# Optimization experiments

Measured on AMD Instinct MI355X. Metric: run time of the kernel, lower is better.

Reference implementation:

```python
import jax, jax.numpy as jnp
import numpy as np

B, L, E, H = 4, 2048, 1024, 16
D = E // H  # head_dim = 64
NEG_INF = -1e9


def _rope(x):
    # x: [B, L, H, D]; standard rotate-half RoPE over head_dim
    seq = x.shape[1]
    inv_freq = 1.0 / (10000.0 ** (jnp.arange(0, D, 2, dtype=jnp.float32) / D))  # [D/2]
    ang = jnp.arange(seq, dtype=jnp.float32)[:, None] * inv_freq               # [L, D/2]
    cos = jnp.concatenate([jnp.cos(ang), jnp.cos(ang)], axis=-1)[None, :, None, :]
    sin = jnp.concatenate([jnp.sin(ang), jnp.sin(ang)], axis=-1)[None, :, None, :]
    x1, x2 = jnp.split(x, 2, axis=-1)
    rot = jnp.concatenate([-x2, x1], axis=-1)
    return x * cos + rot * sin


def setup_inputs() -> dict:
    key = jax.random.key(0)
    ks = jax.random.split(key, 12)
    xavier = lambda k: jax.random.uniform(k, (E, E), jnp.float32,
                                          -np.sqrt(6.0 / (E + E)), np.sqrt(6.0 / (E + E)))
    return {
        "query": jax.random.normal(ks[0], (B, L, E), jnp.float32),
        "key": jax.random.normal(ks[1], (B, L, E), jnp.float32),
        "value": jax.random.normal(ks[2], (B, L, E), jnp.float32),
        "wq": xavier(ks[3]), "bq": jnp.zeros((E,), jnp.float32),
        "wk": xavier(ks[4]), "bk": jnp.zeros((E,), jnp.float32),
        "wv": xavier(ks[5]), "bv": jnp.zeros((E,), jnp.float32),
        "wo": xavier(ks[6]), "bo": jnp.zeros((E,), jnp.float32),
        "key_padding_mask": jax.random.randint(ks[7], (B, L), 0, 2).astype(bool),
    }


def reference(query, key, value, wq, bq, wk, bk, wv, bv, wo, bo, key_padding_mask):
    b, ql = query.shape[0], query.shape[1]
    sl = key.shape[1]
    q = (query @ wq.T + bq).reshape(b, ql, H, D)
    k = (key @ wk.T + bk).reshape(b, sl, H, D)
    v = (value @ wv.T + bv).reshape(b, sl, H, D)
    q = _rope(q)
    k = _rope(k)
    # causal mask (is_causal=True, attn_mask=None path) + key padding mask, additive
    causal = jnp.where(jnp.triu(jnp.ones((ql, sl), bool), k=1), NEG_INF, 0.0)  # [L, L]
    kpm = jnp.where(key_padding_mask[:, None, None, :], NEG_INF, 0.0)          # [B,1,1,S]
    mask = causal[None, None, :, :] + kpm
    scores = jnp.einsum("bqhd,bkhd->bhqk", q, k) / np.sqrt(D) + mask
    attn = jax.nn.softmax(scores, axis=-1)
    out = jnp.einsum("bhqk,bkhd->bqhd", attn, v).reshape(b, ql, E)
    return out @ wo.T + bo
```

## Files before the change

### kernel.cpp

```cpp
#include <hip/hip_runtime.h>

typedef unsigned short u16;
typedef unsigned int   u32;

using bf16x8 = __attribute__((ext_vector_type(8))) __bf16;
using f32x4  = __attribute__((ext_vector_type(4))) float;
using f32x16 = __attribute__((ext_vector_type(16))) float;
using u32x4  = __attribute__((ext_vector_type(4))) u32;

#define DEV static __device__ __forceinline__
#define GP(p) (const __attribute__((address_space(1))) void*)(p)
#define LP(p) (__attribute__((address_space(3))) void*)(p)
#define WAITB(N) asm volatile("s_waitcnt vmcnt(" N ")\n\ts_barrier" ::: "memory")
#define WAITVM(N) do{ asm volatile("s_waitcnt vmcnt(" N ")" ::: "memory"); \
                      __builtin_amdgcn_sched_barrier(0); }while(0)
#define LGKMB asm volatile("s_waitcnt lgkmcnt(0)\n\ts_barrier" ::: "memory")

DEV u16 f2bf(float f){
  u32 u = __builtin_bit_cast(u32, f);
  u32 r = u + 0x7fffu + ((u>>16)&1u);
  return (u16)(r>>16);
}
DEV float bcf(u32 x){ return __builtin_bit_cast(float, x); }
DEV bf16x8 as_bf(uint4 v){ return __builtin_bit_cast(bf16x8, v); }
DEV u32 cvt_pk(float lo, float hi){
  u32 r;
  asm("v_cvt_pk_bf16_f32 %0, %1, %2" : "=v"(r) : "v"(lo), "v"(hi));
  return r;
}
DEV void plswap(u32 &a, u32 &b){
  auto r = __builtin_amdgcn_permlane32_swap((int)a, (int)b, false, false);
  a = (u32)r[0]; b = (u32)r[1];
}
DEV float fexp2(float x){ float r; asm("v_exp_f32 %0, %1" : "=v"(r) : "v"(x)); return r; }
DEV float max3f(float a, float b, float c){
  float r; asm("v_max3_f32 %0, %1, %2, %3" : "=v"(r) : "v"(a), "v"(b), "v"(c)); return r;
}
DEV float fractf_(float x){ float r; asm("v_fract_f32 %0, %1" : "=v"(r) : "v"(x)); return r; }
DEV float sinrev(float f){ float r; asm("v_sin_f32 %0, %1" : "=v"(r) : "v"(f)); return r; }
DEV float cosrev(float f){ float r; asm("v_cos_f32 %0, %1" : "=v"(r) : "v"(f)); return r; }

constexpr int CB = 4, CL = 2048, CE = 1024, CH = 16, CD = 64;
constexpr int CM = CB*CL;
constexpr float LOG2E  = 1.44269504088896f;
constexpr float NEGBIG = -1.44269504e9f;
constexpr float INV2PI = 0.15915494309189535f;

__global__ void mask_kernel(const void* __restrict__ mask, float* __restrict__ maskf){
  __shared__ int a_gt1, a_badf, a_oddnz, a_evennz;
  if (threadIdx.x==0){ a_gt1=0; a_badf=0; a_oddnz=0; a_evennz=0; }
  __syncthreads();
  const u32* w = (const u32*)mask;
  int gt1=0, badf=0, oddnz=0, evennz=0;
  for (int i=threadIdx.x; i<2048; i+=256){
    u32 v = w[i];
    if (v > 1u) gt1 = 1;
    if (v != 0u && v != 0x3f800000u) badf = 1;
    if (v != 0u){ if (i & 1) oddnz = 1; else evennz = 1; }
  }
  if (gt1) atomicOr(&a_gt1,1);
  if (badf) atomicOr(&a_badf,1);
  if (oddnz) atomicOr(&a_oddnz,1);
  if (evennz) atomicOr(&a_evennz,1);
  __syncthreads();
  int mode;
  if (!a_gt1)           mode = (!a_oddnz && a_evennz) ? 3 : 0;
  else if (!a_badf)     mode = 1;
  else                  mode = 2;
  int i = blockIdx.x*blockDim.x + threadIdx.x;
  int v;
  if      (mode==0) v = ((const int*)mask)[i] != 0;
  else if (mode==1) v = ((const float*)mask)[i] != 0.f;
  else if (mode==3) v = ((const int*)mask)[2*i] != 0;
  else              v = ((const unsigned char*)mask)[i] != 0;
  maskf[i] = v ? NEGBIG : 0.f;
}

__global__ void cast_w(const float* __restrict__ wq, const float* __restrict__ wk,
                       const float* __restrict__ wv,
                       u16* __restrict__ oq, u16* __restrict__ ok, u16* __restrict__ ov){
  int i = blockIdx.x*blockDim.x + threadIdx.x;
  int w = i >> 18, j = i & ((1<<18)-1);
  const float* in = (w==0)?wq:(w==1)?wk:wv;
  u16* out = (w==0)?oq:(w==1)?ok:ov;
  float4 a = ((const float4*)in)[j];
  ushort4 h;
  h.x = f2bf(a.x); h.y = f2bf(a.y); h.z = f2bf(a.z); h.w = f2bf(a.w);
  ((ushort4*)out)[j] = h;
}

#define CVTW(dst, lo4, hi4) do{ \
  dst.x = cvt_pk(bcf(lo4.x), bcf(lo4.y)); \
  dst.y = cvt_pk(bcf(lo4.z), bcf(lo4.w)); \
  dst.z = cvt_pk(bcf(hi4.x), bcf(hi4.y)); \
  dst.w = cvt_pk(bcf(hi4.z), bcf(hi4.w)); \
}while(0)

__global__ __launch_bounds__(512) void gemm_qkv(
    const float* __restrict__ query, const float* __restrict__ keyp,
    const float* __restrict__ value,
    const u16* __restrict__ wqb, const u16* __restrict__ wkb, const u16* __restrict__ wvb,
    const float* __restrict__ bq, const float* __restrict__ bk, const float* __restrict__ bv,
    u16* __restrict__ Qp, u16* __restrict__ Kp, u16* __restrict__ Vt)
{
  __shared__ u16 LDSU[65536];
  const int z = blockIdx.y;
  const int tid=threadIdx.x, lane=tid&63, wid=tid>>6;
  const int llo=lane&15, lhi=lane>>4;
  int bid = blockIdx.x;
  int xcd = bid&7, j = bid>>3;
  int mb, nb;
  if (z<2){ mb = xcd*4 + (j>>3); nb = j&7; }
  else    { mb = j&3;  nb = xcd*8 + (j>>2); }
  const int m0 = mb*256, n0 = nb*128;
  const int wr = wid>>1, wc = wid&1;
  const int rswA = llo&7;

  f32x4 acc[4][4] = {};

  auto COMP = [&](const u16* asrc, const u16* bsrc){
    const char* as = (const char*)asrc;
    const char* bs = (const char*)bsrc;
    #pragma unroll
    for (int ks=0; ks<2; ks++){
      bf16x8 af[4], bf_[4];
      #pragma unroll
      for (int mr=0;mr<4;mr++){
        int r = wr*64+mr*16+llo;
        af[mr] = as_bf(*(const uint4*)(as + r*128 + (((ks*4+lhi)^rswA)<<4)));
      }
      #pragma unroll
      for (int nr=0;nr<4;nr++){
        int r = wc*64+nr*16+llo;
        bf_[nr] = as_bf(*(const uint4*)(bs + r*128 + (((ks*4+lhi)^rswA)<<4)));
      }
      #pragma unroll
      for (int mr=0;mr<4;mr++)
        #pragma unroll
        for (int nr=0;nr<4;nr++)
          acc[mr][nr] = __builtin_amdgcn_mfma_f32_16x16x32_bf16(af[mr], bf_[nr], acc[mr][nr], 0,0,0);
    }
  };

  if (z < 2){
    const float* Af = z ? keyp : query;
    const u16*  Wb  = z ? wkb : wqb;
    u16* As0 = &LDSU[0];
    u16* As1 = &LDSU[16384];

    const float* aptr[4]; int aco[4];
    #pragma unroll
    for (int i=0;i<4;i++){
      int c = tid + i*512, row=c>>3, sc=(c&7)^(row&7);
      aptr[i] = Af + (size_t)(m0+row)*CE + sc*8;
      aco[i] = c*8;
    }
    u32x4 A0[8], A1[8];

#define LOADA(T, RA) do{ \
  _Pragma("unroll") \
  for (int i=0;i<4;i++){ \
    asm volatile("global_load_dwordx4 %0, %2, off\n\tglobal_load_dwordx4 %1, %2, off offset:16" \
      : "=&v"(RA[2*i]), "=&v"(RA[2*i+1]) : "v"(aptr[i] + (size_t)(T)*64) : "memory"); \
  } \
}while(0)

#define STAGEB(T, SLOT) do{ \
  _Pragma("unroll") \
  for (int i=0;i<2;i++){ \
    int c = tid + i*512, row=c>>3, sc=(c&7)^(row&7); \
    __builtin_amdgcn_global_load_lds(GP(Wb + (size_t)(n0+row)*CE + (T)*64 + sc*8), \
                                     LP(&LDSU[32768 + (SLOT)*8192 + c*8]), 16, 0, 0); \
  } \
}while(0)

#define WRITEA(DST, RA) do{ \
  _Pragma("unroll") \
  for (int i=0;i<4;i++){ \
    u32x4 w; CVTW(w, RA[2*i], RA[2*i+1]); \
    *(u32x4*)&DST[aco[i]] = w; \
  } \
}while(0)

    LOADA(0, A0); STAGEB(0, 0);
    LOADA(1, A1); STAGEB(1, 1);
    WAITVM("10");
    WRITEA(As0, A0);
    LGKMB;

    #pragma unroll 1
    for (int jj=0; jj<7; jj++){
      const int t = 2*jj;
      LOADA(t+2, A0); STAGEB(t+2, (t+2)&3);
      WAITVM("10");
      WRITEA(As1, A1);
      COMP(As0, &LDSU[32768 + (t&3)*8192]);
      LGKMB;
      LOADA(t+3, A1); STAGEB(t+3, (t+3)&3);
      WAITVM("10");
      WRITEA(As0, A0);
      COMP(As1, &LDSU[32768 + ((t+1)&3)*8192]);
      LGKMB;
    }
    WAITVM("0");
    WRITEA(As1, A1);
    COMP(As0, &LDSU[32768 + 2*8192]);
    LGKMB;
    COMP(As1, &LDSU[32768 + 3*8192]);

#undef LOADA
#undef STAGEB
#undef WRITEA

    const int colbase = n0 + wc*64;
    const float* bias = z ? bk : bq;
    u16* outp = z ? Kp : Qp;
    const float scale = z ? 1.f : 0.125f*LOG2E;
    const int h = colbase >> 6;
    float b1[2], b2[2], invr[2];
    #pragma unroll
    for (int nr=0;nr<2;nr++){
      int j2 = nr*16 + llo;
      b1[nr] = bias[colbase + j2];
      b2[nr] = bias[colbase + j2 + 32];
      invr[nr] = exp2f(-(float)j2 * 0.41524101186092033f) * INV2PI;
    }
    #pragma unroll
    for (int mr=0;mr<4;mr++)
      #pragma unroll
      for (int r=0;r<4;r++){
        int row = m0 + wr*64 + mr*16 + lhi*4 + r;
        int b = row >> 11, l = row & 2047;
        u16* dst = outp + (((size_t)(b*CH + h)*CL + l) << 6);
        #pragma unroll
        for (int nr=0;nr<2;nr++){
          int j2 = nr*16 + llo;
          float x1 = (acc[mr][nr][r]   + b1[nr]) * scale;
          float x2 = (acc[mr][nr+2][r] + b2[nr]) * scale;
          float fr = fractf_((float)l * invr[nr]);
          float sn = sinrev(fr), cs = cosrev(fr);
          dst[j2]      = f2bf(x1*cs - x2*sn);
          dst[j2 + 32] = f2bf(x2*cs + x1*sn);
        }
      }
  } else {
    u16* Bs0 = &LDSU[49152];
    u16* Bs1 = &LDSU[57344];

    const float* bptr[2]; int bco[2];
    #pragma unroll
    for (int i=0;i<2;i++){
      int c = tid + i*512, row=c>>3, sc=(c&7)^(row&7);
      bptr[i] = value + (size_t)(n0+row)*CE + sc*8;
      bco[i] = c*8;
    }
    u32x4 B0[4], B1[4];

#define STAGEA(T, SLOT) do{ \
  _Pragma("unroll") \
  for (int i=0;i<4;i++){ \
    int c = tid + i*512, row=c>>3, sc=(c&7)^(row&7); \
    __builtin_amdgcn_global_load_lds(GP(wvb + (size_t)(m0+row)*CE + (T)*64 + sc*8), \
                                     LP(&LDSU[(SLOT)*16384 + c*8]), 16, 0, 0); \
  } \
}while(0)

#define LOADB(T, RB) do{ \
  _Pragma("unroll") \
  for (int i=0;i<2;i++){ \
    asm volatile("global_load_dwordx4 %0, %2, off\n\tglobal_load_dwordx4 %1, %2, off offset:16" \
      : "=&v"(RB[2*i]), "=&v"(RB[2*i+1]) : "v"(bptr[i] + (size_t)(T)*64) : "memory"); \
  } \
}while(0)

#define WRITEB(DST, RB) do{ \
  _Pragma("unroll") \
  for (int i=0;i<2;i++){ \
    u32x4 w; CVTW(w, RB[2*i], RB[2*i+1]); \
    *(u32x4*)&DST[bco[i]] = w; \
  } \
}while(0)

    STAGEA(0,0); LOADB(0, B0);
    STAGEA(1,1); LOADB(1, B1);
    WAITVM("8");
    WRITEB(Bs0, B0);
    LGKMB;

    #pragma unroll 1
    for (int jj=0; jj<7; jj++){
      const int t = 2*jj;
      STAGEA(t+2, (t+2)%3); LOADB(t+2, B0);
      WAITVM("8");
      WRITEB(Bs1, B1);
      COMP(&LDSU[(t%3)*16384], Bs0);
      LGKMB;
      STAGEA(t+3, (t+3)%3); LOADB(t+3, B1);
      WAITVM("8");
      WRITEB(Bs0, B0);
      COMP(&LDSU[((t+1)%3)*16384], Bs1);
      LGKMB;
    }
    WAITVM("0");
    WRITEB(Bs1, B1);
    COMP(&LDSU[(14%3)*16384], Bs0);
    LGKMB;
    COMP(&LDSU[(15%3)*16384], Bs1);

#undef STAGEA
#undef LOADB
#undef WRITEB

    const int colbase = n0 + wc*64;
    #pragma unroll
    for (int mr=0;mr<4;mr++)
      #pragma unroll
      for (int r=0;r<4;r++){
        int row = m0 + wr*64 + mr*16 + lhi*4 + r;
        float bvv = bv[row];
        #pragma unroll
        for (int nr=0;nr<4;nr++){
          int col = colbase + nr*16 + llo;
          Vt[(size_t)row*CM + col] = f2bf(acc[mr][nr][r] + bvv);
        }
      }
  }
}

__global__ __launch_bounds__(512) void gemm_out(
    const u16* __restrict__ A, const float* __restrict__ Btf,
    const float* __restrict__ bias, float* __restrict__ C)
{
  __shared__ u16 As[3][16384];
  __shared__ u16 Bs[2][8192];
  const int tid=threadIdx.x, lane=tid&63, wid=tid>>6;
  const int llo=lane&15, lhi=lane>>4;
  int bid = blockIdx.x;
  int xcd = bid&7, j = bid>>3;
  const int m0 = (xcd*4 + (j>>3))*256, n0 = (j&7)*128;
  const int wr = wid>>1, wc = wid&1;
  const int rswA = llo&7;

  auto STAGEA = [&](int t, int buf){
    #pragma unroll
    for (int i=0;i<4;i++){
      int c = tid + i*512, row=c>>3, sc=(c&7)^(row&7);
      __builtin_amdgcn_global_load_lds(GP(A + (size_t)(m0+row)*CE + t*64 + sc*8),
                                       LP(&As[buf][c*8]), 16, 0, 0);
    }
  };

  const float* bptr[2]; int bco[2];
  #pragma unroll
  for (int i=0;i<2;i++){
    int c = tid + i*512, row=c>>3, sc=(c&7)^(row&7);
    bptr[i] = Btf + (size_t)(n0+row)*CE + sc*8;
    bco[i] = c*8;
  }
  u32x4 B0[4], B1[4];

#define LOADB(T, RB) do{ \
  _Pragma("unroll") \
  for (int i=0;i<2;i++){ \
    asm volatile("global_load_dwordx4 %0, %2, off\n\tglobal_load_dwordx4 %1, %2, off offset:16" \
      : "=&v"(RB[2*i]), "=&v"(RB[2*i+1]) : "v"(bptr[i] + (size_t)(T)*64) : "memory"); \
  } \
}while(0)

#define WRITEB(BUF, RB) do{ \
  _Pragma("unroll") \
  for (int i=0;i<2;i++){ \
    u32x4 w; CVTW(w, RB[2*i], RB[2*i+1]); \
    *(u32x4*)&Bs[BUF][bco[i]] = w; \
  } \
}while(0)

  f32x4 acc[4][4] = {};

  auto COMP = [&](int abuf, int bbuf){
    const char* as = (const char*)As[abuf];
    const char* bs = (const char*)Bs[bbuf];
    #pragma unroll
    for (int ks=0; ks<2; ks++){
      bf16x8 af[4], bf_[4];
      #pragma unroll
      for (int mr=0;mr<4;mr++){
        int r = wr*64+mr*16+llo;
        af[mr] = as_bf(*(const uint4*)(as + r*128 + (((ks*4+lhi)^rswA)<<4)));
      }
      #pragma unroll
      for (int nr=0;nr<4;nr++){
        int r = wc*64+nr*16+llo;
        bf_[nr] = as_bf(*(const uint4*)(bs + r*128 + (((ks*4+lhi)^rswA)<<4)));
      }
      #pragma unroll
      for (int mr=0;mr<4;mr++)
        #pragma unroll
        for (int nr=0;nr<4;nr++)
          acc[mr][nr] = __builtin_amdgcn_mfma_f32_16x16x32_bf16(af[mr], bf_[nr], acc[mr][nr], 0,0,0);
    }
  };

  STAGEA(0,0); LOADB(0, B0);
  STAGEA(1,1); LOADB(1, B1);
  WAITVM("8");
  WRITEB(0, B0);
  LGKMB;

  #pragma unroll 1
  for (int jj=0; jj<7; jj++){
    const int t = 2*jj;
    STAGEA(t+2, (t+2)%3); LOADB(t+2, B0);
    WAITVM("8");
    WRITEB(1, B1);
    COMP(t%3, 0);
    LGKMB;
    STAGEA(t+3, (t+3)%3); LOADB(t+3, B1);
    WAITVM("8");
    WRITEB(0, B0);
    COMP((t+1)%3, 1);
    LGKMB;
  }
  WAITVM("0");
  WRITEB(1, B1);
  COMP(2, 0);
  LGKMB;
  COMP(0, 1);

#undef LOADB
#undef WRITEB

  #pragma unroll
  for (int mr=0;mr<4;mr++)
    #pragma unroll
    for (int nr=0;nr<4;nr++)
      #pragma unroll
      for (int r=0;r<4;r++){
        int row = m0 + wr*64 + mr*16 + lhi*4 + r;
        int col = n0 + wc*64 + nr*16 + llo;
        C[(size_t)row*CE + col] = acc[mr][nr][r] + bias[col];
      }
}

__global__ __launch_bounds__(256,2) void attn_kernel(
    const u16* __restrict__ Qp, const u16* __restrict__ Kp, const u16* __restrict__ Vt,
    const float* __restrict__ maskf, u16* __restrict__ AO)
{
  __shared__ u16 K_lds[4][4096];
  __shared__ u16 V_lds[4][4096];
  __shared__ float M_lds[2048];
  const int bh = blockIdx.x;
  const int slot = blockIdx.y;
  const int b = bh >> 4, h = bh & 15;
  const int tid=threadIdx.x, lane=tid&63, wid=tid>>6;
  const int l31 = lane&31, hi = lane>>5;
  const u16* Qh = Qp + (size_t)bh*CL*CD;
  const u16* Kh = Kp + (size_t)bh*CL*CD;
  const u16* Vhd = Vt + (size_t)(h*CD)*CM + b*CL;

  #pragma unroll
  for (int i=0;i<2;i++)
    __builtin_amdgcn_global_load_lds(GP(maskf + b*CL + (i*256+tid)*4),
                                     LP(&M_lds[(i*256+tid)*4]), 16, 0, 0);

  auto STAGE = [&](int t, int buf){
    const u16* Ksrc = Kh + t*64*CD;
    const u16* Vsrc = Vhd + t*64;
    #pragma unroll
    for (int i=0;i<2;i++){
      int c = tid + i*256;
      int row = c>>3, sc = c&7;
      int c16 = sc ^ (row&7);
      __builtin_amdgcn_global_load_lds(GP(Ksrc + row*CD + c16*8),
                                       LP(&K_lds[buf][c*8]), 16, 0, 0);
      __builtin_amdgcn_global_load_lds(GP(Vsrc + (size_t)row*CM + c16*8),
                                       LP(&V_lds[buf][c*8]), 16, 0, 0);
    }
  };

  const int rowb = l31*128;
  const int rsw  = (l31&7)<<4;
  const int qts2[2] = {15-slot, slot};

  for (int qi=0; qi<2; qi++){
    const int qt = qts2[qi];
    const int qw0 = qt*128 + wid*32;
    const int qlane = qw0 + l31;

    bf16x8 qf[4];
    #pragma unroll
    for (int c=0;c<4;c++)
      qf[c] = as_bf(*(const uint4*)(Qh + (size_t)qlane*CD + c*16 + hi*8));

    f32x16 o0 = {}, o1 = {};
    float m_r = -3e38f, l_r = 0.f;
    f32x16 sA0, sA1, sB0, sB1;

    const int nt = qt*2 + 2;
    STAGE(0,0); STAGE(1,1);

    auto QK = [&](int t, f32x16& d0, f32x16& d1){
      const char* kb = (const char*)K_lds[t&3];
      f32x16 z0 = {}, z1 = {};
      __builtin_amdgcn_s_setprio(1);
      #pragma unroll
      for (int c=0;c<4;c++){
        int cb = (c*32 + hi*16) ^ rsw;
        bf16x8 k0 = as_bf(*(const uint4*)(kb + rowb + cb));
        bf16x8 k1 = as_bf(*(const uint4*)(kb + 4096 + rowb + cb));
        z0 = __builtin_amdgcn_mfma_f32_32x32x16_bf16(k0, qf[c], z0, 0,0,0);
        z1 = __builtin_amdgcn_mfma_f32_32x32x16_bf16(k1, qf[c], z1, 0,0,0);
      }
      __builtin_amdgcn_s_setprio(0);
      d0 = z0; d1 = z1;
    };

    auto SMPV = [&](int tp, f32x16& s0, f32x16& s1){
      const int kv0 = tp*64;
      const char* vb = (const char*)V_lds[tp&3];

      f32x4 cm[8];
      #pragma unroll
      for (int s2=0;s2<2;s2++)
        #pragma unroll
        for (int g=0; g<4; g++)
          cm[s2*4+g] = *(const f32x4*)&M_lds[kv0 + s2*32 + g*8 + hi*4];

      if (kv0 + 63 > qw0){
        #pragma unroll
        for (int s2=0;s2<2;s2++){
          f32x16& sv = s2 ? s1 : s0;
          #pragma unroll
          for (int reg=0; reg<16; reg++){
            int k = kv0 + s2*32 + (reg&3) + (reg>>2)*8 + hi*4;
            float v = sv[reg] + cm[s2*4+(reg>>2)][reg&3];
            sv[reg] = (k > qlane) ? v + NEGBIG : v;
          }
        }
      } else {
        #pragma unroll
        for (int s2=0;s2<2;s2++){
          f32x16& sv = s2 ? s1 : s0;
          #pragma unroll
          for (int reg=0; reg<16; reg++)
            sv[reg] = sv[reg] + cm[s2*4+(reg>>2)][reg&3];
        }
      }

      f32x16 mx;
      #pragma unroll
      for (int r=0;r<16;r++) mx[r] = fmaxf(s0[r], s1[r]);
      float a0 = max3f(mx[0],mx[1],mx[2]);
      float a1 = max3f(mx[3],mx[4],mx[5]);
      float a2 = max3f(mx[6],mx[7],mx[8]);
      float a3 = max3f(mx[9],mx[10],mx[11]);
      float a4 = max3f(mx[12],mx[13],mx[14]);
      float vmax = fmaxf(max3f(a0,a1,a2), max3f(a3,a4,mx[15]));
      vmax = fmaxf(vmax, __shfl_xor(vmax, 32));

      if (__any(vmax > m_r + 12.0f)){
        float mnew = fmaxf(m_r, vmax);
        float sc = fexp2(m_r - mnew);
        l_r *= sc;
        o0 *= sc; o1 *= sc;
        m_r = mnew;
      }

      #pragma unroll
      for (int r=0;r<16;r++){
        s0[r] = fexp2(s0[r] - m_r);
        s1[r] = fexp2(s1[r] - m_r);
      }
      f32x16 sm = s0 + s1;
      #pragma unroll
      for (int w=8; w>=1; w>>=1)
        #pragma unroll
        for (int r=0;r<w;r++) sm[r] = sm[r] + sm[r+w];
      float rsum = sm[0];
      rsum += __shfl_xor(rsum, 32);
      l_r += rsum;

      u32 w_[16];
      #pragma unroll
      for (int s2=0;s2<2;s2++){
        f32x16& sv = s2 ? s1 : s0;
        #pragma unroll
        for (int c=0;c<2;c++){
          u32 a  = cvt_pk(sv[c*8+0], sv[c*8+1]);
          u32 bb = cvt_pk(sv[c*8+2], sv[c*8+3]);
          u32 cc = cvt_pk(sv[c*8+4], sv[c*8+5]);
          u32 dd = cvt_pk(sv[c*8+6], sv[c*8+7]);
          plswap(a, cc); plswap(bb, dd);
          int base = (s2*2+c)*4;
          w_[base+0]=a; w_[base+1]=bb; w_[base+2]=cc; w_[base+3]=dd;
        }
      }

      __builtin_amdgcn_s_setprio(1);
      #pragma unroll
      for (int kc=0; kc<4; kc++){
        bf16x8 pf = as_bf(make_uint4(w_[kc*4], w_[kc*4+1], w_[kc*4+2], w_[kc*4+3]));
        int cb = (kc*32 + hi*16) ^ rsw;
        bf16x8 v0 = as_bf(*(const uint4*)(vb + rowb + cb));
        bf16x8 v1 = as_bf(*(const uint4*)(vb + 4096 + rowb + cb));
        o0 = __builtin_amdgcn_mfma_f32_32x32x16_bf16(v0, pf, o0, 0,0,0);
        o1 = __builtin_amdgcn_mfma_f32_32x32x16_bf16(v1, pf, o1, 0,0,0);
      }
      __builtin_amdgcn_s_setprio(0);
    };

    WAITB("4");
    if (2 < nt) STAGE(2,2);
    QK(0, sA0, sA1);

    #pragma unroll 1
    for (int jx=0; jx<qt; jx++){
      int t = 2*jx+1;
      WAITB("4");
      if (t+2 < nt) STAGE(t+2,(t+2)&3);
      QK(t, sB0, sB1);
      SMPV(t-1, sA0, sA1);
      t = 2*jx+2;
      WAITB("4");
      if (t+2 < nt) STAGE(t+2,(t+2)&3);
      QK(t, sA0, sA1);
      SMPV(t-1, sB0, sB1);
    }
    WAITB("0");
    QK(nt-1, sB0, sB1);
    SMPV(nt-2, sA0, sA1);
    SMPV(nt-1, sB0, sB1);

    float inv = 1.f / l_r;
    u16* dst = AO + (size_t)(b*CL + qlane)*CE + h*CD;
    #pragma unroll
    for (int mt=0; mt<2; mt++){
      f32x16& ov = mt ? o1 : o0;
      #pragma unroll
      for (int g=0; g<4; g++){
        u32 lo  = cvt_pk(ov[g*4+0]*inv, ov[g*4+1]*inv);
        u32 hi2 = cvt_pk(ov[g*4+2]*inv, ov[g*4+3]*inv);
        *(uint2*)(dst + mt*32 + g*8 + hi*4) = make_uint2(lo, hi2);
      }
    }
    __syncthreads();
  }
}

extern "C" void kernel_launch(void* const* d_in, const int* in_sizes, int n_in,
                              void* d_out, int out_size, void* d_ws, size_t ws_size,
                              hipStream_t stream) {
  const float* query = (const float*)d_in[0];
  const float* key_  = (const float*)d_in[1];
  const float* value = (const float*)d_in[2];
  const float* wq = (const float*)d_in[3];
  const float* bq = (const float*)d_in[4];
  const float* wk = (const float*)d_in[5];
  const float* bk = (const float*)d_in[6];
  const float* wv = (const float*)d_in[7];
  const float* bv = (const float*)d_in[8];
  const float* wo = (const float*)d_in[9];
  const float* bo = (const float*)d_in[10];
  const void*  kpm = d_in[11];

  char* ws = (char*)d_ws;
  constexpr size_t SZ_ME_BF = (size_t)CM*CE*2;
  constexpr size_t OFF_MASKF= 256;
  constexpr size_t OFF_AO   = 65536;
  constexpr size_t OFF_KP   = OFF_AO + SZ_ME_BF;
  constexpr size_t OFF_VT   = OFF_KP + SZ_ME_BF;
  constexpr size_t OFF_QP   = OFF_VT + SZ_ME_BF;

  float* maskf = (float*)(ws + OFF_MASKF);
  u16*  AO  = (u16*)(ws + OFF_AO);
  u16*  Kp  = (u16*)(ws + OFF_KP);
  u16*  Vt  = (u16*)(ws + OFF_VT);
  u16*  Qp  = (u16*)(ws + OFF_QP);

  u16* wqb = AO;
  u16* wkb = AO + (size_t)CE*CE;
  u16* wvb = AO + (size_t)2*CE*CE;

  mask_kernel<<<32,256,0,stream>>>(kpm, maskf);
  cast_w<<<3072,256,0,stream>>>(wq, wk, wv, wqb, wkb, wvb);

  gemm_qkv<<<dim3(256,3),512,0,stream>>>(query, key_, value, wqb, wkb, wvb,
                                         bq, bk, bv, Qp, Kp, Vt);

  attn_kernel<<<dim3(CB*CH, 8),256,0,stream>>>(Qp, Kp, Vt, maskf, AO);

  gemm_out<<<256,512,0,stream>>>(AO, wo, bo, (float*)d_out);
}
```

Before: 188.7 us.

## Deepen QKV GEMM register prefetch to triple buffering and fuse prep kernels

```diff
diff --git a/kernel.cpp b/kernel.cpp
--- a/kernel.cpp
+++ b/kernel.cpp
@@ -46,7 +46,21 @@
 constexpr float NEGBIG = -1.44269504e9f;
 constexpr float INV2PI = 0.15915494309189535f;
 
-__global__ void mask_kernel(const void* __restrict__ mask, float* __restrict__ maskf){
+__global__ void prep_kernel(const float* __restrict__ wq, const float* __restrict__ wk,
+                            const float* __restrict__ wv,
+                            u16* __restrict__ oq, u16* __restrict__ ok, u16* __restrict__ ov,
+                            const void* __restrict__ mask, float* __restrict__ maskf){
+  if (blockIdx.x < 3072){
+    int i = blockIdx.x*blockDim.x + threadIdx.x;
+    int w = i >> 18, j = i & ((1<<18)-1);
+    const float* in = (w==0)?wq:(w==1)?wk:wv;
+    u16* out = (w==0)?oq:(w==1)?ok:ov;
+    float4 a = ((const float4*)in)[j];
+    ushort4 h;
+    h.x = f2bf(a.x); h.y = f2bf(a.y); h.z = f2bf(a.z); h.w = f2bf(a.w);
+    ((ushort4*)out)[j] = h;
+    return;
+  }
   __shared__ int a_gt1, a_badf, a_oddnz, a_evennz;
   if (threadIdx.x==0){ a_gt1=0; a_badf=0; a_oddnz=0; a_evennz=0; }
   __syncthreads();
@@ -67,26 +81,13 @@
   if (!a_gt1)           mode = (!a_oddnz && a_evennz) ? 3 : 0;
   else if (!a_badf)     mode = 1;
   else                  mode = 2;
-  int i = blockIdx.x*blockDim.x + threadIdx.x;
+  int i = (blockIdx.x-3072)*blockDim.x + threadIdx.x;
   int v;
   if      (mode==0) v = ((const int*)mask)[i] != 0;
   else if (mode==1) v = ((const float*)mask)[i] != 0.f;
   else if (mode==3) v = ((const int*)mask)[2*i] != 0;
   else              v = ((const unsigned char*)mask)[i] != 0;
   maskf[i] = v ? NEGBIG : 0.f;
-}
-
-__global__ void cast_w(const float* __restrict__ wq, const float* __restrict__ wk,
-                       const float* __restrict__ wv,
-                       u16* __restrict__ oq, u16* __restrict__ ok, u16* __restrict__ ov){
-  int i = blockIdx.x*blockDim.x + threadIdx.x;
-  int w = i >> 18, j = i & ((1<<18)-1);
-  const float* in = (w==0)?wq:(w==1)?wk:wv;
-  u16* out = (w==0)?oq:(w==1)?ok:ov;
-  float4 a = ((const float4*)in)[j];
-  ushort4 h;
-  h.x = f2bf(a.x); h.y = f2bf(a.y); h.z = f2bf(a.z); h.w = f2bf(a.w);
-  ((ushort4*)out)[j] = h;
 }
 
 #define CVTW(dst, lo4, hi4) do{ \
@@ -155,13 +156,13 @@
       aptr[i] = Af + (size_t)(m0+row)*CE + sc*8;
       aco[i] = c*8;
     }
-    u32x4 A0[8], A1[8];
+    u32x4 S0[8], S1[8], S2[8];
 
 #define LOADA(T, RA) do{ \
   _Pragma("unroll") \
   for (int i=0;i<4;i++){ \
     asm volatile("global_load_dwordx4 %0, %2, off\n\tglobal_load_dwordx4 %1, %2, off offset:16" \
-      : "=&v"(RA[2*i]), "=&v"(RA[2*i+1]) : "v"(aptr[i] + (size_t)(T)*64) : "memory"); \
+      : "=&v"((RA)[2*i]), "=&v"((RA)[2*i+1]) : "v"(aptr[i] + (size_t)(T)*64) : "memory"); \
   } \
 }while(0)
 
@@ -175,42 +176,58 @@
 }while(0)
 
 #define WRITEA(DST, RA) do{ \
+  u16* _d = (DST); \
   _Pragma("unroll") \
   for (int i=0;i<4;i++){ \
-    u32x4 w; CVTW(w, RA[2*i], RA[2*i+1]); \
-    *(u32x4*)&DST[aco[i]] = w; \
+    u32x4 w; CVTW(w, (RA)[2*i], (RA)[2*i+1]); \
+    *(u32x4*)&_d[aco[i]] = w; \
   } \
 }while(0)
 
-    LOADA(0, A0); STAGEB(0, 0);
-    LOADA(1, A1); STAGEB(1, 1);
-    WAITVM("10");
-    WRITEA(As0, A0);
+#define QSTEP(T, SL, SW, WN) do{ \
+  STAGEB((T)+2, ((T)+2)&3); \
+  LOADA((T)+3, SL); \
+  WAITVM(WN); \
+  WRITEA(((((T)+1)&1)?As1:As0), SW); \
+  COMP((((T)&1)?As1:As0), &LDSU[32768 + ((T)&3)*8192]); \
+  LGKMB; \
+}while(0)
+
+    LOADA(0, S0); STAGEB(0, 0); STAGEB(1, 1);
+    LOADA(1, S1); LOADA(2, S2);
+    WAITVM("20");
+    WRITEA(As0, S0);
     LGKMB;
 
-    #pragma unroll 1
-    for (int jj=0; jj<7; jj++){
-      const int t = 2*jj;
-      LOADA(t+2, A0); STAGEB(t+2, (t+2)&3);
-      WAITVM("10");
-      WRITEA(As1, A1);
-      COMP(As0, &LDSU[32768 + (t&3)*8192]);
-      LGKMB;
-      LOADA(t+3, A1); STAGEB(t+3, (t+3)&3);
-      WAITVM("10");
-      WRITEA(As0, A0);
-      COMP(As1, &LDSU[32768 + ((t+1)&3)*8192]);
-      LGKMB;
-    }
-    WAITVM("0");
-    WRITEA(As1, A1);
+    QSTEP(0,  S0, S1, "18");
+    QSTEP(1,  S1, S2, "20");
+    QSTEP(2,  S2, S0, "20");
+    QSTEP(3,  S0, S1, "20");
+    QSTEP(4,  S1, S2, "20");
+    QSTEP(5,  S2, S0, "20");
+    QSTEP(6,  S0, S1, "20");
+    QSTEP(7,  S1, S2, "20");
+    QSTEP(8,  S2, S0, "20");
+    QSTEP(9,  S0, S1, "20");
+    QSTEP(10, S1, S2, "20");
+    QSTEP(11, S2, S0, "20");
+    QSTEP(12, S0, S1, "20");
+    STAGEB(15, 3);
+    WAITVM("12");
+    WRITEA(As0, S2);
+    COMP(As1, &LDSU[32768 + 1*8192]);
+    LGKMB;
+    WAITVM("2");
+    WRITEA(As1, S0);
     COMP(As0, &LDSU[32768 + 2*8192]);
     LGKMB;
+    WAITVM("0");
     COMP(As1, &LDSU[32768 + 3*8192]);
 
 #undef LOADA
 #undef STAGEB
 #undef WRITEA
+#undef QSTEP
 
     const int colbase = n0 + wc*64;
     const float* bias = z ? bk : bq;
@@ -254,7 +271,7 @@
       bptr[i] = value + (size_t)(n0+row)*CE + sc*8;
       bco[i] = c*8;
     }
-    u32x4 B0[4], B1[4];
+    u32x4 R0[4], R1[4], R2[4];
 
 #define STAGEA(T, SLOT) do{ \
   _Pragma("unroll") \
@@ -269,47 +286,64 @@
   _Pragma("unroll") \
   for (int i=0;i<2;i++){ \
     asm volatile("global_load_dwordx4 %0, %2, off\n\tglobal_load_dwordx4 %1, %2, off offset:16" \
-      : "=&v"(RB[2*i]), "=&v"(RB[2*i+1]) : "v"(bptr[i] + (size_t)(T)*64) : "memory"); \
+      : "=&v"((RB)[2*i]), "=&v"((RB)[2*i+1]) : "v"(bptr[i] + (size_t)(T)*64) : "memory"); \
   } \
 }while(0)
 
 #define WRITEB(DST, RB) do{ \
+  u16* _d = (DST); \
   _Pragma("unroll") \
   for (int i=0;i<2;i++){ \
-    u32x4 w; CVTW(w, RB[2*i], RB[2*i+1]); \
-    *(u32x4*)&DST[bco[i]] = w; \
+    u32x4 w; CVTW(w, (RB)[2*i], (RB)[2*i+1]); \
+    *(u32x4*)&_d[bco[i]] = w; \
   } \
 }while(0)
 
-    STAGEA(0,0); LOADB(0, B0);
-    STAGEA(1,1); LOADB(1, B1);
-    WAITVM("8");
-    WRITEB(Bs0, B0);
+#define VSTEP(T, SL, SW, WN) do{ \
+  STAGEA((T)+2, ((T)+2)%3); \
+  LOADB((T)+3, SL); \
+  WAITVM(WN); \
+  WRITEB(((((T)+1)&1)?Bs1:Bs0), SW); \
+  COMP(&LDSU[(((T))%3)*16384], (((T)&1)?Bs1:Bs0)); \
+  LGKMB; \
+}while(0)
+
+    STAGEA(0,0); LOADB(0, R0);
+    STAGEA(1,1); LOADB(1, R1);
+    LOADB(2, R2);
+    WAITVM("12");
+    WRITEB(Bs0, R0);
     LGKMB;
 
-    #pragma unroll 1
-    for (int jj=0; jj<7; jj++){
-      const int t = 2*jj;
-      STAGEA(t+2, (t+2)%3); LOADB(t+2, B0);
-      WAITVM("8");
-      WRITEB(Bs1, B1);
-      COMP(&LDSU[(t%3)*16384], Bs0);
-      LGKMB;
-      STAGEA(t+3, (t+3)%3); LOADB(t+3, B1);
-      WAITVM("8");
-      WRITEB(Bs0, B0);
-      COMP(&LDSU[((t+1)%3)*16384], Bs1);
-      LGKMB;
-    }
+    VSTEP(0,  R0, R1, "12");
+    VSTEP(1,  R1, R2, "16");
+    VSTEP(2,  R2, R0, "16");
+    VSTEP(3,  R0, R1, "16");
+    VSTEP(4,  R1, R2, "16");
+    VSTEP(5,  R2, R0, "16");
+    VSTEP(6,  R0, R1, "16");
+    VSTEP(7,  R1, R2, "16");
+    VSTEP(8,  R2, R0, "16");
+    VSTEP(9,  R0, R1, "16");
+    VSTEP(10, R1, R2, "16");
+    VSTEP(11, R2, R0, "16");
+    VSTEP(12, R0, R1, "16");
+    STAGEA(15, 0);
+    WAITVM("12");
+    WRITEB(Bs0, R2);
+    COMP(&LDSU[1*16384], Bs1);
+    LGKMB;
+    WAITVM("4");
+    WRITEB(Bs1, R0);
+    COMP(&LDSU[2*16384], Bs0);
+    LGKMB;
     WAITVM("0");
-    WRITEB(Bs1, B1);
-    COMP(&LDSU[(14%3)*16384], Bs0);
-    LGKMB;
-    COMP(&LDSU[(15%3)*16384], Bs1);
+    COMP(&LDSU[0*16384], Bs1);
 
 #undef STAGEA
 #undef LOADB
 #undef WRITEB
+#undef VSTEP
 
     const int colbase = n0 + wc*64;
     #pragma unroll
@@ -363,14 +397,14 @@
   _Pragma("unroll") \
   for (int i=0;i<2;i++){ \
     asm volatile("global_load_dwordx4 %0, %2, off\n\tglobal_load_dwordx4 %1, %2, off offset:16" \
-      : "=&v"(RB[2*i]), "=&v"(RB[2*i+1]) : "v"(bptr[i] + (size_t)(T)*64) : "memory"); \
+      : "=&v"((RB)[2*i]), "=&v"((RB)[2*i+1]) : "v"(bptr[i] + (size_t)(T)*64) : "memory"); \
   } \
 }while(0)
 
 #define WRITEB(BUF, RB) do{ \
   _Pragma("unroll") \
   for (int i=0;i<2;i++){ \
-    u32x4 w; CVTW(w, RB[2*i], RB[2*i+1]); \
+    u32x4 w; CVTW(w, (RB)[2*i], (RB)[2*i+1]); \
     *(u32x4*)&Bs[BUF][bco[i]] = w; \
   } \
 }while(0)
@@ -681,8 +715,7 @@
   u16* wkb = AO + (size_t)CE*CE;
   u16* wvb = AO + (size_t)2*CE*CE;
 
-  mask_kernel<<<32,256,0,stream>>>(kpm, maskf);
-  cast_w<<<3072,256,0,stream>>>(wq, wk, wv, wqb, wkb, wvb);
+  prep_kernel<<<3104,256,0,stream>>>(wq, wk, wv, wqb, wkb, wvb, kpm, maskf);
 
   gemm_qkv<<<dim3(256,3),512,0,stream>>>(query, key_, value, wqb, wkb, wvb,
                                          bq, bk, bv, Qp, Kp, Vt);
```

Measured after the change: 180.6 us, median of 3. 1.04x faster.
